# Kernel tuning notes

Measured on AMD Instinct MI355X. Metric: run time of the kernel, lower is better.

## Reference

```python
import jax, jax.numpy as jnp
import numpy as np
from jax import lax

VTH = 0.5
GRAD_WIN = 0.5
CDECAY = 0.5
VDECAY = 0.75

@jax.custom_vjp
def pseudo_spike(v):
    # PseudoSpikeRect: heaviside fwd, rectangular surrogate grad bwd
    return (v > VTH).astype(v.dtype)

def _ps_fwd(v):
    return pseudo_spike(v), v

def _ps_bwd(v, g):
    return (g * (jnp.abs(v - VTH) < GRAD_WIN).astype(g.dtype),)

pseudo_spike.defvjp(_ps_fwd, _ps_bwd)

def conv2d(x, w, b):
    y = lax.conv_general_dilated(x, w, (1, 1), 'VALID',
                                 dimension_numbers=('NCHW', 'OIHW', 'NCHW'))
    return y + b[None, :, None, None]

def lif(psp, state):
    # CUBA-LIF: current decay + integrate, voltage decay with spike reset, threshold
    cur, volt, spk = state
    cur = CDECAY * cur + psp
    volt = VDECAY * volt * (1.0 - spk) + cur
    spk = pseudo_spike(volt)
    return spk, (cur, volt, spk)

def setup_inputs() -> dict:
    key = jax.random.key(0)
    ks = jax.random.split(key, 16)
    B, T = 64, 200
    c1, c2, c3 = 64, 128, 256
    s = lambda k, shape, scale: jax.random.normal(k, shape, jnp.float32) * scale
    return {
        'input_data': jax.random.normal(ks[0], (B, 1, 10, 10, T), jnp.float32),
        'conv1_w': s(ks[1], (c1, 1, 3, 3), 0.3), 'conv1_b': s(ks[2], (c1,), 0.1),
        'conv2_w': s(ks[3], (c2, c1, 3, 3), 0.05), 'conv2_b': s(ks[4], (c2,), 0.1),
        'conv3_w': s(ks[5], (c3, c2, 3, 3), 0.03), 'conv3_b': s(ks[6], (c3,), 0.1),
        'tc_w': s(ks[7], (3, c3, c3), 0.06), 'tc_b': s(ks[8], (3, c3), 0.1),
        'rec_w': s(ks[9], (c3, c3), 0.06), 'rec_b': s(ks[10], (c3,), 0.1),
        'fc1_w': s(ks[11], (128, c3), 0.06), 'fc1_b': s(ks[12], (128,), 0.1),
        'fc2_w': s(ks[13], (2, 128), 0.09),
        'ts_weights': jnp.ones((T, 1), jnp.float32) / T,
    }

def reference(input_data, conv1_w, conv1_b, conv2_w, conv2_b, conv3_w, conv3_b,
              tc_w, tc_b, rec_w, rec_b, fc1_w, fc1_b, fc2_w, ts_weights):
    B = input_data.shape[0]
    c1, c2, c3 = conv1_w.shape[0], conv2_w.shape[0], conv3_w.shape[0]
    f1 = fc1_w.shape[0]

    def zs(shape):
        z = jnp.zeros(shape, input_data.dtype)
        return (z, z, z)

    carry0 = (zs((B, c1, 8, 8)), zs((B, c2, 6, 6)), zs((B, c3, 1, 1)),
              zs((B, c3)), zs((B, c3)), zs((B, f1)),
              jnp.zeros((3, B, c3), input_data.dtype),  # temporal buffer, idx0 = newest
              jnp.int32(0))
    xs = jnp.moveaxis(input_data, -1, 0)  # [T, B, 1, 10, 10]

    def step_fn(carry, xw):
        c1_st, c2_st, c3_st, tc_st, r_st, f_st, buf, step = carry
        x, w = xw
        s1, c1_st = lif(conv2d(x, conv1_w, conv1_b), c1_st)       # [B,c1,8,8]
        s2, c2_st = lif(conv2d(s1, conv2_w, conv2_b), c2_st)      # [B,c2,6,6]
        p = s2.reshape(B, c2, 3, 2, 3, 2).mean(axis=(3, 5))       # AvgPool2d(2) -> [B,c2,3,3]
        s3, c3_st = lif(conv2d(p, conv3_w, conv3_b), c3_st)       # [B,c3,1,1]
        flat = s3.reshape(B, -1)                                   # [B,c3]
        buf = jnp.concatenate([flat[None], buf[:2]], axis=0)
        # temporal conv: tap i applies to spike at time t-i, only if it exists
        psp = jnp.zeros_like(flat)
        for i in range(3):
            tap = buf[i] @ tc_w[i].T + tc_b[i]
            psp = psp + jnp.where(step >= i, 1.0, 0.0).astype(tap.dtype) * tap
        s_tc, tc_st = lif(psp, tc_st)
        # recurrent cell: identity feedforward + linear on previous spike
        psp_r = s_tc + r_st[2] @ rec_w.T + rec_b
        s_r, r_st = lif(psp_r, r_st)
        s_f, f_st = lif(s_r @ fc1_w.T + fc1_b, f_st)
        out = (s_f @ fc2_w.T) * w  # w = ts_weights[step], shape [1]
        return (c1_st, c2_st, c3_st, tc_st, r_st, f_st, buf, step + 1), out

    _, outs = lax.scan(step_fn, carry0, (xs, ts_weights))
    return outs.sum(axis=0)  # [B, 2]
```

## Files before the change

### kernel.cpp

```cpp
#include <hip/hip_runtime.h>


#define B_   64
#define T_   200
#define TCB_ 50

__device__ __forceinline__ void lif32(float psp, float& cur, float& volt, float& spk) {
#pragma clang fp contract(off)
    cur  = __fadd_rn(__fmul_rn(0.5f, cur), psp);
    volt = __fadd_rn(__fmul_rn(__fmul_rn(0.75f, volt), __fsub_rn(1.0f, spk)), cur);
    spk  = (volt > 0.5f) ? 1.0f : 0.0f;
}

__global__ void k_setup(const float* __restrict__ w2, const float* __restrict__ w3,
                        const float* __restrict__ tcw, const float* __restrict__ recw,
                        const float* __restrict__ fw,
                        float* __restrict__ w2T, float* __restrict__ w3T,
                        float* __restrict__ tcT, float* __restrict__ recT,
                        float* __restrict__ fc1T) {
    int idx = blockIdx.x * 256 + threadIdx.x;
    if (idx < 73728) { int o = idx & 127, k = idx >> 7; w2T[idx] = w2[o * 576 + k]; return; }
    idx -= 73728;
    if (idx < 294912) { int o = idx & 255, k = idx >> 8; w3T[idx] = w3[o * 1152 + k]; return; }
    idx -= 294912;
    if (idx < 196608) { int tap = idx >> 16, r = idx & 65535; int o = r & 255, k = r >> 8;
                        tcT[idx] = tcw[tap * 65536 + o * 256 + k]; return; }
    idx -= 196608;
    if (idx < 65536) { int o = idx & 255, k = idx >> 8; recT[idx] = recw[o * 256 + k]; return; }
    idx -= 65536;
    if (idx < 32768) { int o = idx & 127, k = idx >> 7; fc1T[idx] = fw[o * 256 + k]; return; }
}

__global__ __launch_bounds__(256) void k_conv1(const float* __restrict__ x,
                                               const float* __restrict__ w1,
                                               const float* __restrict__ b1,
                                               unsigned char* __restrict__ s1c,
                                               float* __restrict__ st1,
                                               int t0, int TC, int first) {
    int idx = blockIdx.x * 256 + threadIdx.x;
    int xx = idx & 7, yy = (idx >> 3) & 7, o = (idx >> 6) & 63, b = idx >> 12;
    float w[9];
#pragma unroll
    for (int i = 0; i < 9; i++) w[i] = w1[o * 9 + i];
    float bias = b1[o];
    const float* xb = x + (size_t)b * 20000;
    unsigned char* sb = s1c + (size_t)b * TC * 4096 + (o << 6) + (yy << 3) + xx;
    float cur, volt, spk;
    if (first) { cur = 0.f; volt = 0.f; spk = 0.f; }
    else { cur = st1[idx]; volt = st1[262144 + idx]; spk = st1[524288 + idx]; }
    for (int tl = 0; tl < TC; tl += 4) {
        int t = t0 + tl;
        float a0 = 0.f, a1 = 0.f, a2 = 0.f, a3 = 0.f;
#pragma unroll
        for (int i = 0; i < 3; i++) {
#pragma unroll
            for (int j = 0; j < 3; j++) {
                float4 v = *(const float4*)&xb[((yy + i) * 10 + xx + j) * T_ + t];
                float wv = w[i * 3 + j];
                a0 = fmaf(wv, v.x, a0); a1 = fmaf(wv, v.y, a1);
                a2 = fmaf(wv, v.z, a2); a3 = fmaf(wv, v.w, a3);
            }
        }
        float accs[4] = {a0, a1, a2, a3};
#pragma unroll
        for (int q = 0; q < 4; q++) {
            float psp = __fadd_rn(accs[q], bias);
            lif32(psp, cur, volt, spk);
            sb[(size_t)(tl + q) * 4096] = (unsigned char)spk;
        }
    }
    st1[idx] = cur; st1[262144 + idx] = volt; st1[524288 + idx] = spk;
}

__global__ __launch_bounds__(384) void k_conv2(const unsigned char* __restrict__ s1c,
                                               const float* __restrict__ w2T,
                                               const float* __restrict__ b2,
                                               float* __restrict__ psp2c, int TC) {
    __shared__ float s_s[2][4096];
    int blk = blockIdx.x;
    int th = TC >> 1;
    int b = blk / th, tp = blk - b * th;
    int tl0 = 2 * tp;
    int tid = threadIdx.x;
#pragma unroll
    for (int h = 0; h < 2; h++) {
        const unsigned int* src4 = (const unsigned int*)(s1c + (size_t)(b * TC + tl0 + h) * 4096);
        for (int i = tid; i < 1024; i += 384) {
            unsigned int u = src4[i];
            s_s[h][4 * i + 0] = (float)(u & 0xff);
            s_s[h][4 * i + 1] = (float)((u >> 8) & 0xff);
            s_s[h][4 * i + 2] = (float)((u >> 16) & 0xff);
            s_s[h][4 * i + 3] = (float)(u >> 24);
        }
    }
    __syncthreads();
    int oc = tid & 127;
    int yg = tid >> 7;
    int y0 = 2 * yg;
    float a0[2][6], a1[2][6];
#pragma unroll
    for (int h = 0; h < 2; h++)
#pragma unroll
        for (int xq = 0; xq < 6; xq++) { a0[h][xq] = 0.f; a1[h][xq] = 0.f; }
    const float* wb = w2T + oc;
    float w[9];
#pragma unroll
    for (int q = 0; q < 9; q++) w[q] = wb[(size_t)q * 128];
    for (int c = 0; c < 64; c++) {
        int cn = (c + 1) & 63;
        float wn[9];
#pragma unroll
        for (int q = 0; q < 9; q++) wn[q] = wb[(size_t)(cn * 9 + q) * 128];
#pragma unroll
        for (int h = 0; h < 2; h++) {
            const float* sc = &s_s[h][c * 64 + y0 * 8];
            float row[4][8];
#pragma unroll
            for (int ry = 0; ry < 4; ry++) {
                float4 fa = *(const float4*)(sc + ry * 8);
                float4 fb = *(const float4*)(sc + ry * 8 + 4);
                row[ry][0] = fa.x; row[ry][1] = fa.y; row[ry][2] = fa.z; row[ry][3] = fa.w;
                row[ry][4] = fb.x; row[ry][5] = fb.y; row[ry][6] = fb.z; row[ry][7] = fb.w;
            }
#pragma unroll
            for (int i = 0; i < 3; i++)
#pragma unroll
                for (int j = 0; j < 3; j++) {
                    float wv = w[i * 3 + j];
#pragma unroll
                    for (int xq = 0; xq < 6; xq++) {
                        a0[h][xq] = fmaf(wv, row[i][xq + j], a0[h][xq]);
                        a1[h][xq] = fmaf(wv, row[i + 1][xq + j], a1[h][xq]);
                    }
                }
        }
#pragma unroll
        for (int q = 0; q < 9; q++) w[q] = wn[q];
    }
    float bv = b2[oc];
#pragma unroll
    for (int h = 0; h < 2; h++) {
        float* base = psp2c + (size_t)(b * TC + tl0 + h) * 4608;
        float* d0 = base + (size_t)(y0 * 6) * 128 + oc;
        float* d1 = base + (size_t)((y0 + 1) * 6) * 128 + oc;
#pragma unroll
        for (int xq = 0; xq < 6; xq++) {
            d0[(size_t)xq * 128] = __fadd_rn(a0[h][xq], bv);
            d1[(size_t)xq * 128] = __fadd_rn(a1[h][xq], bv);
        }
    }
}

__global__ __launch_bounds__(256) void k_lif2pool(const float* __restrict__ psp2c,
                                                  float* __restrict__ pc,
                                                  float* __restrict__ st2,
                                                  int TC, int first) {
    int idx = blockIdx.x * 256 + threadIdx.x;
    int oc = idx & 127;
    int r = idx >> 7;
    int pos = r % 9;
    int b = r / 9;
    int py = pos / 3, px = pos - py * 3;
    const float* pb = psp2c + (size_t)b * TC * 4608;
    int off00 = ((2 * py) * 6 + 2 * px) * 128 + oc;
    int off01 = ((2 * py) * 6 + 2 * px + 1) * 128 + oc;
    int off10 = ((2 * py + 1) * 6 + 2 * px) * 128 + oc;
    int off11 = ((2 * py + 1) * 6 + 2 * px + 1) * 128 + oc;
    float* pd = pc + (size_t)b * TC * 1152 + oc * 9 + pos;
    float c0, c1, c2, c3, v0, v1, v2, v3, s0, s1, s2, s3;
    if (first) {
        c0 = c1 = c2 = c3 = v0 = v1 = v2 = v3 = s0 = s1 = s2 = s3 = 0.f;
    } else {
        c0 = st2[idx];              c1 = st2[73728 + idx];
        c2 = st2[147456 + idx];     c3 = st2[221184 + idx];
        v0 = st2[294912 + idx];     v1 = st2[368640 + idx];
        v2 = st2[442368 + idx];     v3 = st2[516096 + idx];
        s0 = st2[589824 + idx];     s1 = st2[663552 + idx];
        s2 = st2[737280 + idx];     s3 = st2[811008 + idx];
    }
    for (int tl = 0; tl < TC; tl++) {
        const float* pt = pb + (size_t)tl * 4608;
        float p0 = pt[off00];
        float p1 = pt[off01];
        float p2 = pt[off10];
        float p3 = pt[off11];
        lif32(p0, c0, v0, s0);
        lif32(p1, c1, v1, s1);
        lif32(p2, c2, v2, s2);
        lif32(p3, c3, v3, s3);
        pd[(size_t)tl * 1152] = __fmul_rn(0.25f, __fadd_rn(__fadd_rn(__fadd_rn(s0, s1), s2), s3));
    }
    st2[idx] = c0;           st2[73728 + idx] = c1;
    st2[147456 + idx] = c2;  st2[221184 + idx] = c3;
    st2[294912 + idx] = v0;  st2[368640 + idx] = v1;
    st2[442368 + idx] = v2;  st2[516096 + idx] = v3;
    st2[589824 + idx] = s0;  st2[663552 + idx] = s1;
    st2[737280 + idx] = s2;  st2[811008 + idx] = s3;
}

__global__ __launch_bounds__(256) void k_conv3(const float* __restrict__ pc,
                                               const float* __restrict__ w3T,
                                               const float* __restrict__ b3,
                                               float* __restrict__ psp3c) {
    __shared__ float a_s[4 * 1152];
    int row0 = blockIdx.x * 4;
    int tid = threadIdx.x;
    int oq = tid & 63, mg = tid >> 6;
    for (int idx = tid; idx < 4 * 1152; idx += 256) {
        int m = idx / 1152, k = idx - m * 1152;
        a_s[idx] = pc[(size_t)(row0 + m) * 1152 + k];
    }
    __syncthreads();
    float acc[4] = {0.f, 0.f, 0.f, 0.f};
    const float* as_row = &a_s[mg * 1152];
#pragma unroll 4
    for (int k = 0; k < 1152; k++) {
        float4 wv = *(const float4*)&w3T[(size_t)k * 256 + (oq << 2)];
        float am = as_row[k];
        acc[0] = fmaf(wv.x, am, acc[0]);
        acc[1] = fmaf(wv.y, am, acc[1]);
        acc[2] = fmaf(wv.z, am, acc[2]);
        acc[3] = fmaf(wv.w, am, acc[3]);
    }
    float* dst = psp3c + (size_t)(row0 + mg) * 256 + (oq << 2);
#pragma unroll
    for (int oo = 0; oo < 4; oo++)
        dst[oo] = __fadd_rn(acc[oo], b3[(oq << 2) + oo]);
}

__global__ __launch_bounds__(256) void k_scan3(const float* __restrict__ psp3c,
                                               unsigned char* __restrict__ s3u8,
                                               float* __restrict__ st3,
                                               int t0, int TC, int first) {
    int idx = blockIdx.x * 256 + threadIdx.x;
    int b = idx >> 8, n = idx & 255;
    float cur, volt, spk;
    if (first) { cur = 0.f; volt = 0.f; spk = 0.f; }
    else { cur = st3[idx]; volt = st3[16384 + idx]; spk = st3[32768 + idx]; }
    for (int tl = 0; tl < TC; tl++) {
        lif32(psp3c[(size_t)(b * TC + tl) * 256 + n], cur, volt, spk);
        s3u8[((size_t)b * T_ + t0 + tl) * 256 + n] = (unsigned char)spk;
    }
    st3[idx] = cur; st3[16384 + idx] = volt; st3[32768 + idx] = spk;
}

__global__ __launch_bounds__(256) void k_tc(const unsigned char* __restrict__ s3u8,
                                            const float* __restrict__ tcT,
                                            const float* __restrict__ tc_b,
                                            float* __restrict__ ptcc, int t0) {
    __shared__ float a_s[16 * 256];
    int crow0 = blockIdx.x * 16;
    int tid = threadIdx.x;
    int oq = tid & 63, mg = tid >> 6;
    float psum[4][4];
#pragma unroll
    for (int oo = 0; oo < 4; oo++)
#pragma unroll
        for (int mi = 0; mi < 4; mi++) psum[oo][mi] = 0.f;
    for (int tap = 0; tap < 3; tap++) {
        __syncthreads();
        for (int idx = tid; idx < 16 * 256; idx += 256) {
            int m = idx >> 8, k = idx & 255;
            int crow = crow0 + m;
            int b = crow / TCB_, tl = crow - b * TCB_;
            int t = t0 + tl;
            float v = 0.f;
            if (t >= tap) v = (float)s3u8[((size_t)b * T_ + t - tap) * 256 + k];
            a_s[idx] = v;
        }
        __syncthreads();
        float acc[4][4];
#pragma unroll
        for (int oo = 0; oo < 4; oo++)
#pragma unroll
            for (int mi = 0; mi < 4; mi++) acc[oo][mi] = 0.f;
        const float* wbase = tcT + (size_t)tap * 65536 + (oq << 2);
        for (int k = 0; k < 256; k++) {
            float4 wv = *(const float4*)(wbase + (size_t)k * 256);
            float w4[4] = {wv.x, wv.y, wv.z, wv.w};
            float am[4];
#pragma unroll
            for (int mi = 0; mi < 4; mi++) am[mi] = a_s[(mg * 4 + mi) * 256 + k];
#pragma unroll
            for (int oo = 0; oo < 4; oo++)
#pragma unroll
                for (int mi = 0; mi < 4; mi++)
                    acc[oo][mi] = fmaf(w4[oo], am[mi], acc[oo][mi]);
        }
#pragma unroll
        for (int mi = 0; mi < 4; mi++) {
            int crow = crow0 + mg * 4 + mi;
            int b = crow / TCB_, tl = crow - b * TCB_;
            int t = t0 + tl;
            float g = (t >= tap) ? 1.0f : 0.0f;
#pragma unroll
            for (int oo = 0; oo < 4; oo++) {
                int oc = (oq << 2) + oo;
                float tap_f = __fadd_rn(acc[oo][mi], tc_b[tap * 256 + oc]);
                psum[oo][mi] = __fadd_rn(psum[oo][mi], __fmul_rn(g, tap_f));
            }
        }
    }
#pragma unroll
    for (int mi = 0; mi < 4; mi++) {
        int crow = crow0 + mg * 4 + mi;
        float* dst = ptcc + (size_t)crow * 256 + (oq << 2);
#pragma unroll
        for (int oo = 0; oo < 4; oo++) dst[oo] = psum[oo][mi];
    }
}

__global__ __launch_bounds__(256) void k_scan_tc(const float* __restrict__ ptcc,
                                                 unsigned char* __restrict__ s_tc8,
                                                 float* __restrict__ st_tc,
                                                 int t0, int first) {
    int idx = blockIdx.x * 256 + threadIdx.x;
    int b = idx >> 8, n = idx & 255;
    float cur, volt, spk;
    if (first) { cur = 0.f; volt = 0.f; spk = 0.f; }
    else { cur = st_tc[idx]; volt = st_tc[16384 + idx]; spk = st_tc[32768 + idx]; }
    for (int tl = 0; tl < TCB_; tl++) {
        lif32(ptcc[(size_t)(b * TCB_ + tl) * 256 + n], cur, volt, spk);
        s_tc8[((size_t)b * T_ + t0 + tl) * 256 + n] = (unsigned char)spk;
    }
    st_tc[idx] = cur; st_tc[16384 + idx] = volt; st_tc[32768 + idx] = spk;
}

__global__ __launch_bounds__(512)
__attribute__((amdgpu_waves_per_eu(2, 2)))
void k_rec(const unsigned char* __restrict__ s_tc8,
           const float* __restrict__ rec_w,
           const float* __restrict__ rec_b,
           unsigned char* __restrict__ s_r8) {
    __shared__ __align__(16) float spk_s[2][256];
    __shared__ float acc_s[256];
    int b = blockIdx.x;
    int tid = threadIdx.x;
    int o = tid & 255, half = tid >> 8;
    const float* wrow = rec_w + (size_t)o * 256 + (half << 7);
#define WD(i) float4 w##i = *(const float4*)&wrow[4 * i];
    WD(0)  WD(1)  WD(2)  WD(3)  WD(4)  WD(5)  WD(6)  WD(7)
    WD(8)  WD(9)  WD(10) WD(11) WD(12) WD(13) WD(14) WD(15)
    WD(16) WD(17) WD(18) WD(19) WD(20) WD(21) WD(22) WD(23)
    WD(24) WD(25) WD(26) WD(27) WD(28) WD(29) WD(30) WD(31)
#undef WD
    if (half == 0) spk_s[0][o] = 0.f;
    float cur = 0.f, volt = 0.f, spk = 0.f;
    float rb = rec_b[o];
    const unsigned char* stp = s_tc8 + (size_t)b * T_ * 256 + o;
    unsigned char* srp = s_r8 + (size_t)b * T_ * 256 + o;
    __syncthreads();
    int p = 0;
#define CH(i, sp) { float4 sv = *(const float4*)&(sp)[4 * i]; \
        acc = fmaf(sv.x, w##i.x, acc); acc = fmaf(sv.y, w##i.y, acc); \
        acc = fmaf(sv.z, w##i.z, acc); acc = fmaf(sv.w, w##i.w, acc); }
#define CHAIN32(sp) \
    CH(0,sp)  CH(1,sp)  CH(2,sp)  CH(3,sp)  CH(4,sp)  CH(5,sp)  CH(6,sp)  CH(7,sp) \
    CH(8,sp)  CH(9,sp)  CH(10,sp) CH(11,sp) CH(12,sp) CH(13,sp) CH(14,sp) CH(15,sp) \
    CH(16,sp) CH(17,sp) CH(18,sp) CH(19,sp) CH(20,sp) CH(21,sp) CH(22,sp) CH(23,sp) \
    CH(24,sp) CH(25,sp) CH(26,sp) CH(27,sp) CH(28,sp) CH(29,sp) CH(30,sp) CH(31,sp)
    for (int t = 0; t < T_; t++) {
        if (half == 0) {
            const float* sp = spk_s[p];
            float acc = 0.f;
            CHAIN32(sp)
            acc_s[o] = acc;
        }
        __syncthreads();
        if (half == 1) {
            float stc = (float)stp[(size_t)t * 256];
            const float* sp = spk_s[p] + 128;
            float acc = acc_s[o];
            CHAIN32(sp)
            float psp = __fadd_rn(__fadd_rn(stc, acc), rb);
            lif32(psp, cur, volt, spk);
            srp[(size_t)t * 256] = (unsigned char)spk;
            spk_s[p ^ 1][o] = spk;
        }
        __syncthreads();
        p ^= 1;
    }
#undef CH
#undef CHAIN32
}

__global__ __launch_bounds__(256) void k_fc1(const unsigned char* __restrict__ s_r8,
                                             const float* __restrict__ fc1T,
                                             const float* __restrict__ fc1_b,
                                             float* __restrict__ pfc, int t0) {
    __shared__ float a_s[16 * 256];
    int crow0 = blockIdx.x * 16;
    int tid = threadIdx.x;
    int oq = tid & 31, mg = tid >> 5;
    float acc[4][2];
#pragma unroll
    for (int oo = 0; oo < 4; oo++) { acc[oo][0] = 0.f; acc[oo][1] = 0.f; }
    for (int idx = tid; idx < 16 * 256; idx += 256) {
        int m = idx >> 8, k = idx & 255;
        int crow = crow0 + m;
        int b = crow / TCB_, tl = crow - b * TCB_;
        a_s[idx] = (float)s_r8[((size_t)b * T_ + t0 + tl) * 256 + k];
    }
    __syncthreads();
    for (int k = 0; k < 256; k++) {
        float4 wv = *(const float4*)&fc1T[(size_t)k * 128 + (oq << 2)];
        float w4[4] = {wv.x, wv.y, wv.z, wv.w};
        float a0 = a_s[(mg * 2 + 0) * 256 + k];
        float a1 = a_s[(mg * 2 + 1) * 256 + k];
#pragma unroll
        for (int oo = 0; oo < 4; oo++) {
            acc[oo][0] = fmaf(w4[oo], a0, acc[oo][0]);
            acc[oo][1] = fmaf(w4[oo], a1, acc[oo][1]);
        }
    }
#pragma unroll
    for (int mi = 0; mi < 2; mi++) {
        float* dst = pfc + (size_t)(crow0 + mg * 2 + mi) * 128 + (oq << 2);
#pragma unroll
        for (int oo = 0; oo < 4; oo++)
            dst[oo] = __fadd_rn(acc[oo][mi], fc1_b[(oq << 2) + oo]);
    }
}

__global__ __launch_bounds__(256) void k_scan_f(const float* __restrict__ pfc,
                                                unsigned char* __restrict__ s_f8,
                                                float* __restrict__ st_f,
                                                int t0, int first) {
    int idx = blockIdx.x * 256 + threadIdx.x;
    int b = idx >> 7, n = idx & 127;
    float cur, volt, spk;
    if (first) { cur = 0.f; volt = 0.f; spk = 0.f; }
    else { cur = st_f[idx]; volt = st_f[8192 + idx]; spk = st_f[16384 + idx]; }
    for (int tl = 0; tl < TCB_; tl++) {
        lif32(pfc[(size_t)(b * TCB_ + tl) * 128 + n], cur, volt, spk);
        s_f8[((size_t)b * T_ + t0 + tl) * 128 + n] = (unsigned char)spk;
    }
    st_f[idx] = cur; st_f[8192 + idx] = volt; st_f[16384 + idx] = spk;
}

__global__ __launch_bounds__(128) void k_final(const unsigned char* __restrict__ s_f8,
                                               const float* __restrict__ ts,
                                               const float* __restrict__ fc2,
                                               float* __restrict__ out) {
    __shared__ double q_s[128];
    int b = blockIdx.x, k = threadIdx.x;
    double q = 0.0;
    const unsigned char* sf = s_f8 + (size_t)b * T_ * 128 + k;
    for (int t = 0; t < T_; t++) q = fma((double)ts[t], (double)sf[(size_t)t * 128], q);
    q_s[k] = q;
    __syncthreads();
    if (k < 2) {
        double o = 0.0;
        for (int kk = 0; kk < 128; kk++) o = fma((double)fc2[k * 128 + kk], q_s[kk], o);
        out[b * 2 + k] = (float)o;
    }
}

extern "C" void kernel_launch(void* const* d_in, const int* in_sizes, int n_in,
                              void* d_out, int out_size, void* d_ws, size_t ws_size,
                              hipStream_t stream) {
    const float* x       = (const float*)d_in[0];
    const float* conv1_w = (const float*)d_in[1];
    const float* conv1_b = (const float*)d_in[2];
    const float* conv2_w = (const float*)d_in[3];
    const float* conv2_b = (const float*)d_in[4];
    const float* conv3_w = (const float*)d_in[5];
    const float* conv3_b = (const float*)d_in[6];
    const float* tc_w    = (const float*)d_in[7];
    const float* tc_b    = (const float*)d_in[8];
    const float* rec_w   = (const float*)d_in[9];
    const float* rec_b   = (const float*)d_in[10];
    const float* fc1_w   = (const float*)d_in[11];
    const float* fc1_b   = (const float*)d_in[12];
    const float* fc2_w   = (const float*)d_in[13];
    const float* ts_w    = (const float*)d_in[14];
    float* out = (float*)d_out;
    (void)in_sizes; (void)n_in; (void)out_size;

    char* base = (char*)d_ws;
    float* w2T  = (float*)(base + 0);
    float* w3T  = (float*)(base + 294912);
    float* tcT  = (float*)(base + 1474560);
    float* recT = (float*)(base + 2260992);
    float* fc1T = (float*)(base + 2523136);
    float* st1  = (float*)(base + 2654208);
    float* st2  = (float*)(base + 5799936);
    float* st3  = (float*)(base + 9338880);
    float* st_tc= (float*)(base + 9535488);
    float* st_f = (float*)(base + 9732096);
    unsigned char* s3u8  = (unsigned char*)(base + 9830400);
    unsigned char* s_tc8 = (unsigned char*)(base + 13107200);
    unsigned char* s_r8  = (unsigned char*)(base + 16384000);
    unsigned char* s_f8  = (unsigned char*)(base + 19660800);

    const size_t PERS = 21299200;
    const size_t PER_T = 1802240;
    int TCF;
    if      (ws_size >= PERS + 40 * PER_T) TCF = 40;
    else if (ws_size >= PERS + 20 * PER_T) TCF = 20;
    else if (ws_size >= PERS +  8 * PER_T) TCF = 8;
    else                                   TCF = 4;
    int NCH = T_ / TCF;
    char* cb = base + PERS;
    float* psp2c = (float*)(cb);
    float* psp3c = (float*)(cb + (size_t)TCF * 1179648);
    float* pc    = (float*)(cb + (size_t)TCF * (1179648 + 65536));
    unsigned char* s1c = (unsigned char*)(cb + (size_t)TCF * (1179648 + 65536 + 294912));
    float* ptcc = (float*)(cb);
    float* pfc  = (float*)(cb + 3276800);

    k_setup<<<2592, 256, 0, stream>>>(conv2_w, conv3_w, tc_w, rec_w, fc1_w,
                                      w2T, w3T, tcT, recT, fc1T);
    for (int ch = 0; ch < NCH; ch++) {
        int t0 = ch * TCF;
        int first = (ch == 0) ? 1 : 0;
        k_conv1<<<1024, 256, 0, stream>>>(x, conv1_w, conv1_b, s1c, st1, t0, TCF, first);
        k_conv2<<<B_ * TCF / 2, 384, 0, stream>>>(s1c, w2T, conv2_b, psp2c, TCF);
        k_lif2pool<<<288, 256, 0, stream>>>(psp2c, pc, st2, TCF, first);
        k_conv3<<<B_ * TCF / 4, 256, 0, stream>>>(pc, w3T, conv3_b, psp3c);
        k_scan3<<<64, 256, 0, stream>>>(psp3c, s3u8, st3, t0, TCF, first);
    }
    for (int bc = 0; bc < T_ / TCB_; bc++) {
        int t0 = bc * TCB_;
        k_tc<<<B_ * TCB_ / 16, 256, 0, stream>>>(s3u8, tcT, tc_b, ptcc, t0);
        k_scan_tc<<<64, 256, 0, stream>>>(ptcc, s_tc8, st_tc, t0, (bc == 0) ? 1 : 0);
    }
    k_rec<<<64, 512, 0, stream>>>(s_tc8, rec_w, rec_b, s_r8);
    for (int bc = 0; bc < T_ / TCB_; bc++) {
        int t0 = bc * TCB_;
        k_fc1<<<B_ * TCB_ / 16, 256, 0, stream>>>(s_r8, fc1T, fc1_b, pfc, t0);
        k_scan_f<<<32, 256, 0, stream>>>(pfc, s_f8, st_f, t0, (bc == 0) ? 1 : 0);
    }
    k_final<<<64, 128, 0, stream>>>(s_f8, ts_w, fc2_w, out);
}
```

Before: 2.397 ms.

## Restructure conv2 so each thread computes a full 6x6 output tile per timestep

The conv2 kernel changes from blocks of 384 threads covering two timesteps, with each thread doing two output rows, to blocks of 128 threads covering one timestep, with each thread accumulating the entire 6x6 output map for one output channel. Each weight load and each shared-memory row read is now reused across more outputs. Weight prefetching for the next channel is dropped. The 36 accumulators plus 64 row values raise register pressure and may reduce occupancy, and the grid doubles in block count while each block shrinks.

```diff
diff --git a/kernel.cpp b/kernel.cpp
--- a/kernel.cpp
+++ b/kernel.cpp
@@ -72,83 +72,61 @@
     st1[idx] = cur; st1[262144 + idx] = volt; st1[524288 + idx] = spk;
 }
 
-__global__ __launch_bounds__(384) void k_conv2(const unsigned char* __restrict__ s1c,
+__global__ __launch_bounds__(128) void k_conv2(const unsigned char* __restrict__ s1c,
                                                const float* __restrict__ w2T,
                                                const float* __restrict__ b2,
                                                float* __restrict__ psp2c, int TC) {
-    __shared__ float s_s[2][4096];
+    __shared__ float s_s[4096];
     int blk = blockIdx.x;
-    int th = TC >> 1;
-    int b = blk / th, tp = blk - b * th;
-    int tl0 = 2 * tp;
     int tid = threadIdx.x;
-#pragma unroll
-    for (int h = 0; h < 2; h++) {
-        const unsigned int* src4 = (const unsigned int*)(s1c + (size_t)(b * TC + tl0 + h) * 4096);
-        for (int i = tid; i < 1024; i += 384) {
-            unsigned int u = src4[i];
-            s_s[h][4 * i + 0] = (float)(u & 0xff);
-            s_s[h][4 * i + 1] = (float)((u >> 8) & 0xff);
-            s_s[h][4 * i + 2] = (float)((u >> 16) & 0xff);
-            s_s[h][4 * i + 3] = (float)(u >> 24);
-        }
+    const unsigned int* src4 = (const unsigned int*)(s1c + (size_t)blk * 4096);
+    for (int i = tid; i < 1024; i += 128) {
+        unsigned int u = src4[i];
+        s_s[4 * i + 0] = (float)(u & 0xff);
+        s_s[4 * i + 1] = (float)((u >> 8) & 0xff);
+        s_s[4 * i + 2] = (float)((u >> 16) & 0xff);
+        s_s[4 * i + 3] = (float)(u >> 24);
     }
     __syncthreads();
-    int oc = tid & 127;
-    int yg = tid >> 7;
-    int y0 = 2 * yg;
-    float a0[2][6], a1[2][6];
-#pragma unroll
-    for (int h = 0; h < 2; h++)
-#pragma unroll
-        for (int xq = 0; xq < 6; xq++) { a0[h][xq] = 0.f; a1[h][xq] = 0.f; }
+    int oc = tid;
+    float acc[6][6];
+#pragma unroll
+    for (int y = 0; y < 6; y++)
+#pragma unroll
+        for (int x = 0; x < 6; x++) acc[y][x] = 0.f;
     const float* wb = w2T + oc;
-    float w[9];
-#pragma unroll
-    for (int q = 0; q < 9; q++) w[q] = wb[(size_t)q * 128];
     for (int c = 0; c < 64; c++) {
-        int cn = (c + 1) & 63;
-        float wn[9];
-#pragma unroll
-        for (int q = 0; q < 9; q++) wn[q] = wb[(size_t)(cn * 9 + q) * 128];
-#pragma unroll
-        for (int h = 0; h < 2; h++) {
-            const float* sc = &s_s[h][c * 64 + y0 * 8];
-            float row[4][8];
-#pragma unroll
-            for (int ry = 0; ry < 4; ry++) {
-                float4 fa = *(const float4*)(sc + ry * 8);
-                float4 fb = *(const float4*)(sc + ry * 8 + 4);
-                row[ry][0] = fa.x; row[ry][1] = fa.y; row[ry][2] = fa.z; row[ry][3] = fa.w;
-                row[ry][4] = fb.x; row[ry][5] = fb.y; row[ry][6] = fb.z; row[ry][7] = fb.w;
+        float w[9];
+#pragma unroll
+        for (int q = 0; q < 9; q++) w[q] = wb[(size_t)(c * 9 + q) * 128];
+        const float* sc = &s_s[c * 64];
+        float row[8][8];
+#pragma unroll
+        for (int ry = 0; ry < 8; ry++) {
+            float4 fa = *(const float4*)(sc + ry * 8);
+            float4 fb = *(const float4*)(sc + ry * 8 + 4);
+            row[ry][0] = fa.x; row[ry][1] = fa.y; row[ry][2] = fa.z; row[ry][3] = fa.w;
+            row[ry][4] = fb.x; row[ry][5] = fb.y; row[ry][6] = fb.z; row[ry][7] = fb.w;
+        }
+#pragma unroll
+        for (int i = 0; i < 3; i++)
+#pragma unroll
+            for (int j = 0; j < 3; j++) {
+                float wv = w[i * 3 + j];
+#pragma unroll
+                for (int y = 0; y < 6; y++)
+#pragma unroll
+                    for (int x = 0; x < 6; x++)
+                        acc[y][x] = fmaf(wv, row[y + i][x + j], acc[y][x]);
             }
-#pragma unroll
-            for (int i = 0; i < 3; i++)
-#pragma unroll
-                for (int j = 0; j < 3; j++) {
-                    float wv = w[i * 3 + j];
-#pragma unroll
-                    for (int xq = 0; xq < 6; xq++) {
-                        a0[h][xq] = fmaf(wv, row[i][xq + j], a0[h][xq]);
-                        a1[h][xq] = fmaf(wv, row[i + 1][xq + j], a1[h][xq]);
-                    }
-                }
-        }
-#pragma unroll
-        for (int q = 0; q < 9; q++) w[q] = wn[q];
     }
     float bv = b2[oc];
-#pragma unroll
-    for (int h = 0; h < 2; h++) {
-        float* base = psp2c + (size_t)(b * TC + tl0 + h) * 4608;
-        float* d0 = base + (size_t)(y0 * 6) * 128 + oc;
-        float* d1 = base + (size_t)((y0 + 1) * 6) * 128 + oc;
-#pragma unroll
-        for (int xq = 0; xq < 6; xq++) {
-            d0[(size_t)xq * 128] = __fadd_rn(a0[h][xq], bv);
-            d1[(size_t)xq * 128] = __fadd_rn(a1[h][xq], bv);
-        }
-    }
+    float* base = psp2c + (size_t)blk * 4608 + oc;
+#pragma unroll
+    for (int y = 0; y < 6; y++)
+#pragma unroll
+        for (int x = 0; x < 6; x++)
+            base[(size_t)(y * 6 + x) * 128] = __fadd_rn(acc[y][x], bv);
 }
 
 __global__ __launch_bounds__(256) void k_lif2pool(const float* __restrict__ psp2c,
@@ -515,7 +493,7 @@
         int t0 = ch * TCF;
         int first = (ch == 0) ? 1 : 0;
         k_conv1<<<1024, 256, 0, stream>>>(x, conv1_w, conv1_b, s1c, st1, t0, TCF, first);
-        k_conv2<<<B_ * TCF / 2, 384, 0, stream>>>(s1c, w2T, conv2_b, psp2c, TCF);
+        k_conv2<<<B_ * TCF, 128, 0, stream>>>(s1c, w2T, conv2_b, psp2c, TCF);
         k_lif2pool<<<288, 256, 0, stream>>>(psp2c, pc, st2, TCF, first);
         k_conv3<<<B_ * TCF / 4, 256, 0, stream>>>(pc, w3T, conv3_b, psp3c);
         k_scan3<<<64, 256, 0, stream>>>(psp3c, s3u8, st3, t0, TCF, first);
```

Result: faster. 2.261 ms (-5.7%).
